# Optimization experiments

Measured on AMD Instinct MI355X. Metric: run time of the kernel, lower is better.

Reference implementation:

```python
import jax, jax.numpy as jnp
import numpy as np

KE = 14.3996454784255
P = 6  # polynomial cutoff order
A_EXP = 0.3
A_PREFACTOR = 0.4543
C = jnp.array([0.1818, 0.5099, 0.2802, 0.02817], dtype=jnp.float32)
K = jnp.array([3.2, 0.9423, 0.4028, 0.2016], dtype=jnp.float32)

N_NODES = 100000
N_EDGES = 6400000
N_ELEM = 10
N_RADII = 119


def setup_inputs() -> dict:
    key = jax.random.key(0)
    k1, k2, k3, k4, k5 = jax.random.split(key, 5)
    # edge distances in a physically plausible range (avoid x ~ 0 -> 1/x blowup)
    x = jax.random.uniform(k1, (N_EDGES, 1), dtype=jnp.float32) * 4.0 + 0.05
    node_attrs = jax.random.uniform(k2, (N_NODES, N_ELEM), dtype=jnp.float32)
    edge_index = jax.random.randint(k3, (2, N_EDGES), 0, N_NODES, dtype=jnp.int64)
    atomic_numbers = jax.random.randint(k4, (N_ELEM,), 1, N_RADII, dtype=jnp.int64)
    # covalent radii table (stand-in for ase.data.covalent_radii), ~0.3..2.6 Angstrom
    covalent_radii = 0.3 + 2.3 * jax.random.uniform(k5, (N_RADII,), dtype=jnp.float32)
    return {
        "x": x,
        "node_attrs": node_attrs,
        "edge_index": edge_index,
        "atomic_numbers": atomic_numbers,
        "covalent_radii": covalent_radii,
    }


def _envelope(x, r_max, p):
    r = x / r_max
    env = (1.0
           - (p + 1.0) * (p + 2.0) / 2.0 * r ** p
           + p * (p + 2.0) * r ** (p + 1)
           - p * (p + 1.0) / 2.0 * r ** (p + 2))
    return env * (x < r_max)


def reference(x, node_attrs, edge_index, atomic_numbers, covalent_radii):
    sender = edge_index[0]    # [E]
    receiver = edge_index[1]  # [E]
    # per-node atomic number from one-hot-ish node_attrs
    node_Z = atomic_numbers[jnp.argmax(node_attrs, axis=1)][:, None]  # [N,1] int
    Z_u = node_Z[sender]   # [E,1] int
    Z_v = node_Z[receiver] # [E,1] int
    Zu_f = Z_u.astype(x.dtype)
    Zv_f = Z_v.astype(x.dtype)
    a = A_PREFACTOR * 0.529 / (Zu_f ** A_EXP + Zv_f ** A_EXP)  # [E,1]
    r_over_a = x / a
    phi = (C[0] * jnp.exp(-K[0] * r_over_a)
           + C[1] * jnp.exp(-K[1] * r_over_a)
           + C[2] * jnp.exp(-K[2] * r_over_a)
           + C[3] * jnp.exp(-K[3] * r_over_a))
    v_edges = KE * Zu_f * Zv_f / x * phi  # [E,1]
    r_max = covalent_radii[Z_u[:, 0]][:, None] + covalent_radii[Z_v[:, 0]][:, None]  # [E,1]
    env = _envelope(x, r_max, float(P))
    v_edges = 0.5 * v_edges * env
    V_ZBL = jax.ops.segment_sum(v_edges, receiver, num_segments=node_attrs.shape[0])  # [N,1]
    return V_ZBL[:, 0]
```

## Files before the change

### kernel.cpp

```cpp
#include <hip/hip_runtime.h>

#define KE_CONST 14.3996454784255f

#define P2_SHIFT 15
#define P2_CHUNK 32768
#define SCAN_B2  64
#define SCAN_THR 1024
#define MAXC     4
#define MAXE     16
#define ELEM_CAP 131072
#define DN_THR   1024
#define DN_BLOCKS 256

__global__ void zbl_prep_elem(const float* __restrict__ node_attrs,
                              unsigned char* __restrict__ elem,
                              int n_nodes, int n_elem) {
    int n = blockIdx.x * blockDim.x + threadIdx.x;
    if (n >= n_nodes) return;
    const float* row = node_attrs + (size_t)n * n_elem;
    float best = row[0];
    int bi = 0;
    for (int i = 1; i < n_elem; ++i) {
        float v = row[i];
        if (v > best) { best = v; bi = i; }
    }
    elem[n] = (unsigned char)bi;
}

__global__ void zbl_prep_pairs(const int* __restrict__ atomic_numbers,
                               const float* __restrict__ covalent_radii,
                               float4* __restrict__ pair_tab,
                               int n_elem) {
    int t = threadIdx.x;
    int np = n_elem * n_elem;
    if (t >= np) return;
    int eu = t / n_elem;
    int ev = t - eu * n_elem;
    int Zu = atomic_numbers[eu];
    int Zv = atomic_numbers[ev];
    float zu = (float)Zu, zv = (float)Zv;
    float inv_a = (__powf(zu, 0.3f) + __powf(zv, 0.3f)) * (1.0f / (0.4543f * 0.529f));
    float kezz  = 0.5f * KE_CONST * zu * zv;
    float rmax  = covalent_radii[Zu] + covalent_radii[Zv];
    pair_tab[t] = make_float4(inv_a, kezz, rmax, 1.0f / rmax);
}

__device__ __forceinline__ unsigned enc_val_p(float xv, const float4& p) {
    float t = xv * p.x;
    float phi = 0.1818f  * __expf(-3.2f    * t)
              + 0.5099f  * __expf(-0.9423f * t)
              + 0.2802f  * __expf(-0.4028f * t)
              + 0.02817f * __expf(-0.2016f * t);
    float rr = xv * p.w;
    float r2 = rr * rr;
    float r6 = r2 * r2 * r2;
    float env = 1.0f - 28.0f * r6 + 48.0f * r6 * rr - 21.0f * r6 * r2;
    float val = fmaxf(p.y * phi / xv * env, 0.0f);
    unsigned e = (__float_as_uint(val) + 0x8000u) >> 16;
    if (e > 0x7FFFu) e = 0x7FFFu;
    return (xv < p.z) ? e : 0u;
}

__global__ __launch_bounds__(DN_THR)
void zbl_dense_lds(const float* __restrict__ x,
                   const int* __restrict__ ei,
                   const unsigned char* __restrict__ elem_g,
                   const float4* __restrict__ pair_tab,
                   unsigned* __restrict__ packed,
                   int n_edges, int n_elem, int n_nodes) {
    __shared__ __align__(16) unsigned char elem[ELEM_CAP];
    __shared__ float4 pt[MAXE * MAXE];

    int np = n_elem * n_elem;
    for (int i = threadIdx.x; i < np; i += DN_THR) pt[i] = pair_tab[i];
    int nwords = (n_nodes + 15) >> 4;
    const uint4* eg4 = (const uint4*)elem_g;
    uint4* el4 = (uint4*)elem;
    for (int i = threadIdx.x; i < nwords; i += DN_THR) el4[i] = eg4[i];
    __syncthreads();

    long long e0 = (((long long)blockIdx.x * n_edges) / DN_BLOCKS) & ~3LL;
    long long e1 = (blockIdx.x == DN_BLOCKS - 1)
                     ? (long long)n_edges
                     : ((((long long)(blockIdx.x + 1) * n_edges) / DN_BLOCKS) & ~3LL);
    long long vend = e1 & ~3LL;

    for (long long b = e0 + (long long)threadIdx.x * 4; b + 4 <= vend;
         b += (long long)DN_THR * 4) {
        int4   s4 = *(const int4*)(ei + b);
        int4   r4 = *(const int4*)(ei + n_edges + b);
        float4 x4 = *(const float4*)(x + b);
        unsigned es0 = elem[s4.x], es1 = elem[s4.y], es2 = elem[s4.z], es3 = elem[s4.w];
        unsigned er0 = elem[r4.x], er1 = elem[r4.y], er2 = elem[r4.z], er3 = elem[r4.w];
        float4 p0 = pt[es0 * n_elem + er0];
        float4 p1 = pt[es1 * n_elem + er1];
        float4 p2 = pt[es2 * n_elem + er2];
        float4 p3 = pt[es3 * n_elem + er3];
        uint4 o;
        o.x = ((unsigned)r4.x << 15) | enc_val_p(x4.x, p0);
        o.y = ((unsigned)r4.y << 15) | enc_val_p(x4.y, p1);
        o.z = ((unsigned)r4.z << 15) | enc_val_p(x4.z, p2);
        o.w = ((unsigned)r4.w << 15) | enc_val_p(x4.w, p3);
        *(uint4*)(packed + b) = o;
    }
    for (long long e = vend + threadIdx.x; e < e1; e += DN_THR) {
        int r = ei[n_edges + e];
        float4 p = pt[elem[ei[e]] * n_elem + elem[r]];
        packed[e] = ((unsigned)r << 15) | enc_val_p(x[e], p);
    }
}

#define SCAN_PROC(P)                                                            \
    if (((P).x >> 30) == c) atomicAdd(&acc[((P).x >> 15) & (P2_CHUNK - 1)],     \
                                      __uint_as_float(((P).x & 0x7FFFu) << 16));\
    if (((P).y >> 30) == c) atomicAdd(&acc[((P).y >> 15) & (P2_CHUNK - 1)],     \
                                      __uint_as_float(((P).y & 0x7FFFu) << 16));\
    if (((P).z >> 30) == c) atomicAdd(&acc[((P).z >> 15) & (P2_CHUNK - 1)],     \
                                      __uint_as_float(((P).z & 0x7FFFu) << 16));\
    if (((P).w >> 30) == c) atomicAdd(&acc[((P).w >> 15) & (P2_CHUNK - 1)],     \
                                      __uint_as_float(((P).w & 0x7FFFu) << 16));

__global__ __launch_bounds__(SCAN_THR)
void zbl_scan(const unsigned* __restrict__ packed,
              float* __restrict__ partial,
              int n_edges) {
    unsigned c = blockIdx.x >> 6;
    int      j = blockIdx.x & (SCAN_B2 - 1);

    __shared__ __align__(16) float acc[P2_CHUNK];
    for (int i = threadIdx.x * 4; i < P2_CHUNK; i += SCAN_THR * 4)
        *(float4*)&acc[i] = make_float4(0.f, 0.f, 0.f, 0.f);
    __syncthreads();

    long long e0 = (((long long)j * n_edges) / SCAN_B2) & ~3LL;
    long long e1 = (j == SCAN_B2 - 1) ? (long long)n_edges
                                      : ((((long long)(j + 1) * n_edges) / SCAN_B2) & ~3LL);

    const long long T4 = (long long)SCAN_THR * 4;
    long long niter = (e1 - e0) / (T4 * 4);
    long long base = e0 + (long long)threadIdx.x * 4;
    for (long long i = 0; i < niter; ++i, base += T4 * 4) {
        uint4 q0 = *(const uint4*)(packed + base);
        uint4 q1 = *(const uint4*)(packed + base + T4);
        uint4 q2 = *(const uint4*)(packed + base + 2 * T4);
        uint4 q3 = *(const uint4*)(packed + base + 3 * T4);
        SCAN_PROC(q0);
        SCAN_PROC(q1);
        SCAN_PROC(q2);
        SCAN_PROC(q3);
    }
    long long rem0 = e0 + niter * T4 * 4;
    long long vend = e1 & ~3LL;
    for (long long b = rem0 + (long long)threadIdx.x * 4; b + 4 <= vend; b += T4) {
        uint4 p = *(const uint4*)(packed + b);
        SCAN_PROC(p);
    }
    for (long long e = vend + threadIdx.x; e < e1; e += SCAN_THR) {
        unsigned w = packed[e];
        if ((w >> 30) == c) atomicAdd(&acc[(w >> 15) & (P2_CHUNK - 1)],
                                      __uint_as_float((w & 0x7FFFu) << 16));
    }

    __syncthreads();
    float* pp = partial + (size_t)blockIdx.x * P2_CHUNK;
    for (int i = threadIdx.x * 4; i < P2_CHUNK; i += SCAN_THR * 4)
        *(float4*)(pp + i) = *(const float4*)&acc[i];
}

__global__ void zbl_reduce(const float* __restrict__ partial,
                           float* __restrict__ out,
                           int n_nodes) {
    int i = blockIdx.x * blockDim.x + threadIdx.x;
    if (i >= n_nodes) return;
    int c  = i >> P2_SHIFT;
    int li = i & (P2_CHUNK - 1);
    const float* p = partial + ((size_t)c * SCAN_B2) * P2_CHUNK + li;
    float s0 = 0.f, s1 = 0.f, s2 = 0.f, s3 = 0.f;
    #pragma unroll
    for (int j = 0; j < SCAN_B2; j += 4) {
        s0 += p[(size_t)(j + 0) * P2_CHUNK];
        s1 += p[(size_t)(j + 1) * P2_CHUNK];
        s2 += p[(size_t)(j + 2) * P2_CHUNK];
        s3 += p[(size_t)(j + 3) * P2_CHUNK];
    }
    out[i] = (s0 + s1) + (s2 + s3);
}

__global__ void zbl_node_prep(const float* __restrict__ node_attrs,
                              const int* __restrict__ atomic_numbers,
                              const float* __restrict__ covalent_radii,
                              float4* __restrict__ node_data,
                              float* __restrict__ out_zero,
                              int n_nodes, int n_elem) {
    int n = blockIdx.x * blockDim.x + threadIdx.x;
    if (n >= n_nodes) return;
    const float* row = node_attrs + (size_t)n * n_elem;
    float best = row[0];
    int bi = 0;
    for (int i = 1; i < n_elem; ++i) {
        float v = row[i];
        if (v > best) { best = v; bi = i; }
    }
    int Z = atomic_numbers[bi];
    float zf = (float)Z;
    node_data[n] = make_float4(zf, __powf(zf, 0.3f), covalent_radii[Z], 0.0f);
    out_zero[n] = 0.0f;
}

__global__ void zbl_edge_atomic(const float* __restrict__ x,
                                const int* __restrict__ edge_index,
                                const float4* __restrict__ node_data,
                                float* __restrict__ out,
                                int n_edges) {
    int e = blockIdx.x * blockDim.x + threadIdx.x;
    if (e >= n_edges) return;
    int snd = edge_index[e];
    int r = edge_index[n_edges + e];
    float xv = x[e];
    float4 du = node_data[snd];
    float4 dv = node_data[r];
    float rmax = du.z + dv.z;
    if (xv >= rmax) return;
    const float inv_a_pref = 1.0f / (0.4543f * 0.529f);
    float t = xv * (du.y + dv.y) * inv_a_pref;
    float phi = 0.1818f  * __expf(-3.2f    * t)
              + 0.5099f  * __expf(-0.9423f * t)
              + 0.2802f  * __expf(-0.4028f * t)
              + 0.02817f * __expf(-0.2016f * t);
    float v = KE_CONST * du.x * dv.x * phi / xv;
    float rr = xv / rmax;
    float r2 = rr * rr;
    float r6 = r2 * r2 * r2;
    float env = 1.0f - 28.0f * r6 + 48.0f * r6 * rr - 21.0f * r6 * r2;
    atomicAdd(&out[r], 0.5f * v * env);
}

extern "C" void kernel_launch(void* const* d_in, const int* in_sizes, int n_in,
                              void* d_out, int out_size, void* d_ws, size_t ws_size,
                              hipStream_t stream) {
    const float* x              = (const float*)d_in[0];
    const float* node_attrs     = (const float*)d_in[1];
    const int*   edge_index     = (const int*)d_in[2];
    const int*   atomic_numbers = (const int*)d_in[3];
    const float* covalent_radii = (const float*)d_in[4];
    float* out = (float*)d_out;

    int n_edges = in_sizes[0];
    int n_elem  = in_sizes[3];
    int n_nodes = in_sizes[1] / n_elem;

    int C = (n_nodes + P2_CHUNK - 1) >> P2_SHIFT;
    size_t elem_bytes   = (((size_t)n_nodes) + 255) & ~(size_t)255;
    size_t pair_bytes   = ((size_t)MAXE * MAXE * sizeof(float4) + 255) & ~(size_t)255;
    size_t packed_bytes = (((size_t)n_edges * sizeof(unsigned)) + 255) & ~(size_t)255;
    size_t part_bytes   = (size_t)C * SCAN_B2 * P2_CHUNK * sizeof(float);
    bool fast = (C >= 1) && (C <= MAXC) && (n_nodes <= ELEM_CAP) &&
                (n_elem >= 1) && (n_elem <= MAXE) &&
                (ws_size >= elem_bytes + pair_bytes + packed_bytes + part_bytes);

    if (fast) {
        unsigned char* elem     = (unsigned char*)d_ws;
        float4*        pair_tab = (float4*)((char*)d_ws + elem_bytes);
        unsigned*      packed   = (unsigned*)((char*)d_ws + elem_bytes + pair_bytes);
        float*         part     = (float*)((char*)d_ws + elem_bytes + pair_bytes + packed_bytes);

        zbl_prep_elem<<<(n_nodes + 255) / 256, 256, 0, stream>>>(
            node_attrs, elem, n_nodes, n_elem);
        zbl_prep_pairs<<<1, 256, 0, stream>>>(
            atomic_numbers, covalent_radii, pair_tab, n_elem);

        zbl_dense_lds<<<DN_BLOCKS, DN_THR, 0, stream>>>(
            x, edge_index, elem, pair_tab, packed, n_edges, n_elem, n_nodes);

        zbl_scan<<<C * SCAN_B2, SCAN_THR, 0, stream>>>(packed, part, n_edges);

        zbl_reduce<<<(n_nodes + 255) / 256, 256, 0, stream>>>(part, out, n_nodes);
        return;
    }

    float4* node_data = (float4*)d_ws;
    zbl_node_prep<<<(n_nodes + 255) / 256, 256, 0, stream>>>(
        node_attrs, atomic_numbers, covalent_radii, node_data,
        out, n_nodes, n_elem);
    zbl_edge_atomic<<<(n_edges + 255) / 256, 256, 0, stream>>>(
        x, edge_index, node_data, out, n_edges);
}
```

Before: 168.5 us.

## Bucket packed edges by node chunk so scan blocks read only their chunk

Adds a counting pass that histograms receivers into node chunks and computes per-block output offsets. The edge kernel then scatters packed (local index, bf16 value) words into chunk-contiguous buckets via shared-memory atomic counters. The scan kernel then reads only its own chunk's segment instead of re-reading and filtering all edges once per chunk. This trades one extra pass over receivers and contended LDS atomics for removing the redundant multi-chunk reads.

```diff
diff --git a/kernel.cpp b/kernel.cpp
--- a/kernel.cpp
+++ b/kernel.cpp
@@ -11,6 +11,7 @@
 #define ELEM_CAP 131072
 #define DN_THR   1024
 #define DN_BLOCKS 256
+#define CNT_THR  1024
 
 __global__ void zbl_prep_elem(const float* __restrict__ node_attrs,
                               unsigned char* __restrict__ elem,
@@ -30,8 +31,10 @@
 __global__ void zbl_prep_pairs(const int* __restrict__ atomic_numbers,
                                const float* __restrict__ covalent_radii,
                                float4* __restrict__ pair_tab,
+                               unsigned* __restrict__ gcount,
                                int n_elem) {
     int t = threadIdx.x;
+    if (t < MAXC) gcount[t] = 0u;
     int np = n_elem * n_elem;
     if (t >= np) return;
     int eu = t / n_elem;
@@ -45,7 +48,59 @@
     pair_tab[t] = make_float4(inv_a, kezz, rmax, 1.0f / rmax);
 }
 
-__device__ __forceinline__ unsigned enc_val_p(float xv, const float4& p) {
+#define CNT4(V)                                                         \
+    { unsigned cc;                                                      \
+      cc = ((unsigned)(V).x) >> P2_SHIFT; c0 += (cc==0); c1 += (cc==1); c2 += (cc==2); c3 += (cc==3); \
+      cc = ((unsigned)(V).y) >> P2_SHIFT; c0 += (cc==0); c1 += (cc==1); c2 += (cc==2); c3 += (cc==3); \
+      cc = ((unsigned)(V).z) >> P2_SHIFT; c0 += (cc==0); c1 += (cc==1); c2 += (cc==2); c3 += (cc==3); \
+      cc = ((unsigned)(V).w) >> P2_SHIFT; c0 += (cc==0); c1 += (cc==1); c2 += (cc==2); c3 += (cc==3); }
+
+__global__ __launch_bounds__(CNT_THR)
+void zbl_count(const int* __restrict__ ei,
+               unsigned* __restrict__ gcount,
+               unsigned* __restrict__ blkpos,
+               int n_edges) {
+    __shared__ unsigned h[MAXC];
+    if (threadIdx.x < MAXC) h[threadIdx.x] = 0u;
+    __syncthreads();
+
+    long long e0 = (((long long)blockIdx.x * n_edges) / DN_BLOCKS) & ~3LL;
+    long long e1 = (blockIdx.x == DN_BLOCKS - 1)
+                     ? (long long)n_edges
+                     : ((((long long)(blockIdx.x + 1) * n_edges) / DN_BLOCKS) & ~3LL);
+    const int* r = ei + n_edges;
+    unsigned c0 = 0, c1 = 0, c2 = 0, c3 = 0;
+
+    const long long T4 = (long long)CNT_THR * 4;
+    long long vend  = e1 & ~3LL;
+    long long niter = (e1 - e0) / (T4 * 4);
+    long long base  = e0 + (long long)threadIdx.x * 4;
+    for (long long i = 0; i < niter; ++i, base += T4 * 4) {
+        int4 a = *(const int4*)(r + base);
+        int4 b = *(const int4*)(r + base + T4);
+        int4 c = *(const int4*)(r + base + 2 * T4);
+        int4 d = *(const int4*)(r + base + 3 * T4);
+        CNT4(a); CNT4(b); CNT4(c); CNT4(d);
+    }
+    long long rem0 = e0 + niter * T4 * 4;
+    for (long long b4 = rem0 + (long long)threadIdx.x * 4; b4 + 4 <= vend; b4 += T4) {
+        int4 a = *(const int4*)(r + b4);
+        CNT4(a);
+    }
+    for (long long e = vend + threadIdx.x; e < e1; e += CNT_THR) {
+        unsigned cc = ((unsigned)r[e]) >> P2_SHIFT;
+        c0 += (cc == 0); c1 += (cc == 1); c2 += (cc == 2); c3 += (cc == 3);
+    }
+
+    atomicAdd(&h[0], c0); atomicAdd(&h[1], c1);
+    atomicAdd(&h[2], c2); atomicAdd(&h[3], c3);
+    __syncthreads();
+    if (threadIdx.x < MAXC)
+        blkpos[blockIdx.x * MAXC + threadIdx.x] =
+            atomicAdd(&gcount[threadIdx.x], h[threadIdx.x]);
+}
+
+__device__ __forceinline__ unsigned enc_val16(float xv, const float4& p) {
     float t = xv * p.x;
     float phi = 0.1818f  * __expf(-3.2f    * t)
               + 0.5099f  * __expf(-0.9423f * t)
@@ -57,26 +112,44 @@
     float env = 1.0f - 28.0f * r6 + 48.0f * r6 * rr - 21.0f * r6 * r2;
     float val = fmaxf(p.y * phi / xv * env, 0.0f);
     unsigned e = (__float_as_uint(val) + 0x8000u) >> 16;
-    if (e > 0x7FFFu) e = 0x7FFFu;
     return (xv < p.z) ? e : 0u;
 }
+
+#define SCATTER(RW, XV, PP)                                                   \
+    { unsigned rr_  = (unsigned)(RW);                                         \
+      unsigned ccx  = rr_ >> P2_SHIFT;                                        \
+      unsigned w_   = ((rr_ & (P2_CHUNK - 1)) << 16) | enc_val16((XV), (PP)); \
+      unsigned sb_  = (ccx == 0) ? seg0 : (ccx == 1) ? seg1                   \
+                    : (ccx == 2) ? seg2 : seg3;                               \
+      unsigned pos_ = atomicAdd(&cur[ccx], 1u);                               \
+      packedB[(size_t)sb_ + pos_] = w_; }
 
 __global__ __launch_bounds__(DN_THR)
 void zbl_dense_lds(const float* __restrict__ x,
                    const int* __restrict__ ei,
                    const unsigned char* __restrict__ elem_g,
                    const float4* __restrict__ pair_tab,
-                   unsigned* __restrict__ packed,
+                   const unsigned* __restrict__ gcount,
+                   const unsigned* __restrict__ blkpos,
+                   unsigned* __restrict__ packedB,
                    int n_edges, int n_elem, int n_nodes) {
     __shared__ __align__(16) unsigned char elem[ELEM_CAP];
     __shared__ float4 pt[MAXE * MAXE];
-
+    __shared__ unsigned cur[MAXC];
+
+    if (threadIdx.x < MAXC) cur[threadIdx.x] = 0u;
     int np = n_elem * n_elem;
     for (int i = threadIdx.x; i < np; i += DN_THR) pt[i] = pair_tab[i];
     int nwords = (n_nodes + 15) >> 4;
     const uint4* eg4 = (const uint4*)elem_g;
     uint4* el4 = (uint4*)elem;
     for (int i = threadIdx.x; i < nwords; i += DN_THR) el4[i] = eg4[i];
+
+    unsigned g0 = gcount[0], g1 = gcount[1], g2 = gcount[2];
+    unsigned seg0 = blkpos[blockIdx.x * MAXC + 0];
+    unsigned seg1 = g0 + blkpos[blockIdx.x * MAXC + 1];
+    unsigned seg2 = g0 + g1 + blkpos[blockIdx.x * MAXC + 2];
+    unsigned seg3 = g0 + g1 + g2 + blkpos[blockIdx.x * MAXC + 3];
     __syncthreads();
 
     long long e0 = (((long long)blockIdx.x * n_edges) / DN_BLOCKS) & ~3LL;
@@ -96,69 +169,69 @@
         float4 p1 = pt[es1 * n_elem + er1];
         float4 p2 = pt[es2 * n_elem + er2];
         float4 p3 = pt[es3 * n_elem + er3];
-        uint4 o;
-        o.x = ((unsigned)r4.x << 15) | enc_val_p(x4.x, p0);
-        o.y = ((unsigned)r4.y << 15) | enc_val_p(x4.y, p1);
-        o.z = ((unsigned)r4.z << 15) | enc_val_p(x4.z, p2);
-        o.w = ((unsigned)r4.w << 15) | enc_val_p(x4.w, p3);
-        *(uint4*)(packed + b) = o;
+        SCATTER(r4.x, x4.x, p0);
+        SCATTER(r4.y, x4.y, p1);
+        SCATTER(r4.z, x4.z, p2);
+        SCATTER(r4.w, x4.w, p3);
     }
     for (long long e = vend + threadIdx.x; e < e1; e += DN_THR) {
         int r = ei[n_edges + e];
         float4 p = pt[elem[ei[e]] * n_elem + elem[r]];
-        packed[e] = ((unsigned)r << 15) | enc_val_p(x[e], p);
-    }
-}
-
-#define SCAN_PROC(P)                                                            \
-    if (((P).x >> 30) == c) atomicAdd(&acc[((P).x >> 15) & (P2_CHUNK - 1)],     \
-                                      __uint_as_float(((P).x & 0x7FFFu) << 16));\
-    if (((P).y >> 30) == c) atomicAdd(&acc[((P).y >> 15) & (P2_CHUNK - 1)],     \
-                                      __uint_as_float(((P).y & 0x7FFFu) << 16));\
-    if (((P).z >> 30) == c) atomicAdd(&acc[((P).z >> 15) & (P2_CHUNK - 1)],     \
-                                      __uint_as_float(((P).z & 0x7FFFu) << 16));\
-    if (((P).w >> 30) == c) atomicAdd(&acc[((P).w >> 15) & (P2_CHUNK - 1)],     \
-                                      __uint_as_float(((P).w & 0x7FFFu) << 16));
+        float xv = x[e];
+        SCATTER(r, xv, p);
+    }
+}
+
+#define ACC1(W) atomicAdd(&acc[(W) >> 16], __uint_as_float(((W) & 0xFFFFu) << 16))
+#define ACC4(Q) { ACC1((Q).x); ACC1((Q).y); ACC1((Q).z); ACC1((Q).w); }
 
 __global__ __launch_bounds__(SCAN_THR)
-void zbl_scan(const unsigned* __restrict__ packed,
-              float* __restrict__ partial,
-              int n_edges) {
+void zbl_scan_b(const unsigned* __restrict__ packedB,
+                const unsigned* __restrict__ gcount,
+                float* __restrict__ partial,
+                int n_edges) {
     unsigned c = blockIdx.x >> 6;
     int      j = blockIdx.x & (SCAN_B2 - 1);
 
     __shared__ __align__(16) float acc[P2_CHUNK];
     for (int i = threadIdx.x * 4; i < P2_CHUNK; i += SCAN_THR * 4)
         *(float4*)&acc[i] = make_float4(0.f, 0.f, 0.f, 0.f);
-    __syncthreads();
-
-    long long e0 = (((long long)j * n_edges) / SCAN_B2) & ~3LL;
-    long long e1 = (j == SCAN_B2 - 1) ? (long long)n_edges
-                                      : ((((long long)(j + 1) * n_edges) / SCAN_B2) & ~3LL);
-
+
+    unsigned g0 = gcount[0], g1 = gcount[1], g2 = gcount[2], g3 = gcount[3];
+    long long cst = (c == 0) ? 0LL
+                  : (c == 1) ? (long long)g0
+                  : (c == 2) ? (long long)g0 + g1
+                             : (long long)g0 + g1 + g2;
+    long long cnt = (c == 0) ? (long long)g0
+                  : (c == 1) ? (long long)g1
+                  : (c == 2) ? (long long)g2 : (long long)g3;
+    long long s = cst + cnt * j / SCAN_B2;
+    long long e = cst + cnt * (j + 1) / SCAN_B2;
+    __syncthreads();
+
+    long long va = (s + 3) & ~3LL; if (va > e) va = e;
+    long long ve = e & ~3LL;       if (ve < va) ve = va;
+
+    for (long long i = s + threadIdx.x; i < va; i += SCAN_THR) {
+        unsigned w = packedB[i]; ACC1(w);
+    }
     const long long T4 = (long long)SCAN_THR * 4;
-    long long niter = (e1 - e0) / (T4 * 4);
-    long long base = e0 + (long long)threadIdx.x * 4;
+    long long niter = (ve - va) / (T4 * 4);
+    long long base  = va + (long long)threadIdx.x * 4;
     for (long long i = 0; i < niter; ++i, base += T4 * 4) {
-        uint4 q0 = *(const uint4*)(packed + base);
-        uint4 q1 = *(const uint4*)(packed + base + T4);
-        uint4 q2 = *(const uint4*)(packed + base + 2 * T4);
-        uint4 q3 = *(const uint4*)(packed + base + 3 * T4);
-        SCAN_PROC(q0);
-        SCAN_PROC(q1);
-        SCAN_PROC(q2);
-        SCAN_PROC(q3);
-    }
-    long long rem0 = e0 + niter * T4 * 4;
-    long long vend = e1 & ~3LL;
-    for (long long b = rem0 + (long long)threadIdx.x * 4; b + 4 <= vend; b += T4) {
-        uint4 p = *(const uint4*)(packed + b);
-        SCAN_PROC(p);
-    }
-    for (long long e = vend + threadIdx.x; e < e1; e += SCAN_THR) {
-        unsigned w = packed[e];
-        if ((w >> 30) == c) atomicAdd(&acc[(w >> 15) & (P2_CHUNK - 1)],
-                                      __uint_as_float((w & 0x7FFFu) << 16));
+        uint4 q0 = *(const uint4*)(packedB + base);
+        uint4 q1 = *(const uint4*)(packedB + base + T4);
+        uint4 q2 = *(const uint4*)(packedB + base + 2 * T4);
+        uint4 q3 = *(const uint4*)(packedB + base + 3 * T4);
+        ACC4(q0); ACC4(q1); ACC4(q2); ACC4(q3);
+    }
+    long long rem0 = va + niter * T4 * 4;
+    for (long long b = rem0 + (long long)threadIdx.x * 4; b + 4 <= ve; b += T4) {
+        uint4 q = *(const uint4*)(packedB + b);
+        ACC4(q);
+    }
+    for (long long i = ve + threadIdx.x; i < e; i += SCAN_THR) {
+        unsigned w = packedB[i]; ACC1(w);
     }
 
     __syncthreads();
@@ -252,27 +325,34 @@
     int C = (n_nodes + P2_CHUNK - 1) >> P2_SHIFT;
     size_t elem_bytes   = (((size_t)n_nodes) + 255) & ~(size_t)255;
     size_t pair_bytes   = ((size_t)MAXE * MAXE * sizeof(float4) + 255) & ~(size_t)255;
+    size_t meta_bytes   = (((size_t)(MAXC + DN_BLOCKS * MAXC) * 4) + 255) & ~(size_t)255;
     size_t packed_bytes = (((size_t)n_edges * sizeof(unsigned)) + 255) & ~(size_t)255;
     size_t part_bytes   = (size_t)C * SCAN_B2 * P2_CHUNK * sizeof(float);
     bool fast = (C >= 1) && (C <= MAXC) && (n_nodes <= ELEM_CAP) &&
-                (n_elem >= 1) && (n_elem <= MAXE) &&
-                (ws_size >= elem_bytes + pair_bytes + packed_bytes + part_bytes);
+                (n_elem >= 1) && (n_elem <= MAXE) && ((n_edges & 3) == 0) &&
+                (ws_size >= elem_bytes + pair_bytes + meta_bytes + packed_bytes + part_bytes);
 
     if (fast) {
         unsigned char* elem     = (unsigned char*)d_ws;
         float4*        pair_tab = (float4*)((char*)d_ws + elem_bytes);
-        unsigned*      packed   = (unsigned*)((char*)d_ws + elem_bytes + pair_bytes);
-        float*         part     = (float*)((char*)d_ws + elem_bytes + pair_bytes + packed_bytes);
-
+        unsigned*      gcount   = (unsigned*)((char*)d_ws + elem_bytes + pair_bytes);
+        unsigned*      blkpos   = gcount + 8;
+        unsigned*      packedB  = (unsigned*)((char*)d_ws + elem_bytes + pair_bytes + meta_bytes);
+        float*         part     = (float*)((char*)d_ws + elem_bytes + pair_bytes + meta_bytes + packed_bytes);
+
+        zbl_prep_pairs<<<1, 256, 0, stream>>>(
+            atomic_numbers, covalent_radii, pair_tab, gcount, n_elem);
         zbl_prep_elem<<<(n_nodes + 255) / 256, 256, 0, stream>>>(
             node_attrs, elem, n_nodes, n_elem);
-        zbl_prep_pairs<<<1, 256, 0, stream>>>(
-            atomic_numbers, covalent_radii, pair_tab, n_elem);
+
+        zbl_count<<<DN_BLOCKS, CNT_THR, 0, stream>>>(
+            edge_index, gcount, blkpos, n_edges);
 
         zbl_dense_lds<<<DN_BLOCKS, DN_THR, 0, stream>>>(
-            x, edge_index, elem, pair_tab, packed, n_edges, n_elem, n_nodes);
-
-        zbl_scan<<<C * SCAN_B2, SCAN_THR, 0, stream>>>(packed, part, n_edges);
+            x, edge_index, elem, pair_tab, gcount, blkpos, packedB,
+            n_edges, n_elem, n_nodes);
+
+        zbl_scan_b<<<C * SCAN_B2, SCAN_THR, 0, stream>>>(packedB, gcount, part, n_edges);
 
         zbl_reduce<<<(n_nodes + 255) / 256, 256, 0, stream>>>(part, out, n_nodes);
         return;
```

Result: slower. 193.8 us (+15.0%).
